# Kernel tuning notes

Hardware: AMD Instinct MI355X
Metric: run time of the kernel (lower is better)

## Reference

```python
import jax, jax.numpy as jnp
import numpy as np

BATCH, K_DIM, SEQ_L = 8, 1, 2048
D_MODEL, D_STATE, KCH = 256, 64, 2  # 64 complex states == d_state 128 real; 2 kernel channels (bidirectional)


def setup_inputs() -> dict:
    key = jax.random.key(0)
    ks = jax.random.split(key, 12)
    H, N = D_MODEL, D_STATE
    s = 1.0 / np.sqrt(H)
    # log-uniform timestep in [1e-3, 1e-1] as in S4 init
    dt = jnp.exp(jax.random.uniform(ks[2], (H,)) * (np.log(0.1) - np.log(0.001)) + np.log(0.001))
    return {
        "x": jax.random.normal(ks[0], (BATCH, H, K_DIM, SEQ_L), jnp.float32),
        "t": jax.random.normal(ks[1], (BATCH, 1, H), jnp.float32),
        "W_t": jax.random.normal(ks[3], (H, H)) * s,
        "b_t": jnp.zeros((H,)),
        "ln_g": jnp.ones((H,)),
        "ln_b": jnp.zeros((H,)),
        "log_dt": jnp.log(dt),
        "log_A_real": jnp.log(0.5 * jnp.ones((H, N))),
        "A_imag": jnp.tile(np.pi * jnp.arange(N, dtype=np.float32), (H, 1)),
        "B_re": jnp.ones((H, N)),
        "B_im": jnp.zeros((H, N)),
        "C_re": jax.random.normal(ks[4], (KCH, H, N)) * np.sqrt(0.5),
        "C_im": jax.random.normal(ks[5], (KCH, H, N)) * np.sqrt(0.5),
        "D": jax.random.normal(ks[6], (H,)),
        "W_out": jax.random.normal(ks[7], (H, H)) * s,
        "b_out": jnp.zeros((H,)),
        "W1": jax.random.normal(ks[8], (H, H)) * s,
        "b1": jnp.zeros((H,)),
        "W2": jax.random.normal(ks[9], (H, H)) * s,
        "b2": jnp.zeros((H,)),
    }


def _s4_kernel(log_dt, log_A_real, A_imag, B_re, B_im, C_re, C_im, L):
    # Diagonal SSM convolution kernel (ZOH discretization), 2 channels for bidirectional
    dt = jnp.exp(log_dt)[:, None]                      # (H,1)
    A = -jnp.exp(log_A_real) + 1j * A_imag             # (H,N)
    B = B_re + 1j * B_im                               # (H,N)
    C = C_re + 1j * C_im                               # (KCH,H,N)
    dtA = dt * A
    dB = B * (jnp.exp(dtA) - 1.0) / A                  # ZOH input discretization
    V = jnp.exp(dtA[:, :, None] * jnp.arange(L))       # (H,N,L) Vandermonde of dA^l
    return 2.0 * jnp.einsum('chn,hnl->chl', C * dB, V).real  # (KCH,H,L)


def _s4_layer(u, ln_g, ln_b, log_dt, log_A_real, A_imag, B_re, B_im, C_re, C_im, D, W_out, b_out):
    # u: (B*, H, L). Pre-LayerNorm over channels, S4 FFT conv, D skip, GELU, out proj, residual.
    mu = jnp.mean(u, axis=1, keepdims=True)
    var = jnp.var(u, axis=1, keepdims=True)
    z = (u - mu) / jnp.sqrt(var + 1e-5) * ln_g[:, None] + ln_b[:, None]
    L = u.shape[-1]
    k = _s4_kernel(log_dt, log_A_real, A_imag, B_re, B_im, C_re, C_im, L)
    # bidirectional: causal kernel + time-reversed kernel, combined at length 2L
    k_bi = jnp.pad(k[0], ((0, 0), (0, L))) + jnp.pad(k[1][:, ::-1], ((0, 0), (L, 0)))  # (H,2L)
    kf = jnp.fft.rfft(k_bi, n=2 * L)                   # (H,L+1)
    zf = jnp.fft.rfft(z, n=2 * L)                      # (B*,H,L+1)
    y = jnp.fft.irfft(zf * kf[None], n=2 * L)[..., :L]
    y = y + z * D[:, None]
    y = jax.nn.gelu(y, approximate=False)
    y = jnp.einsum('oh,bhl->bol', W_out, y) + b_out[:, None]  # transposed output linear
    return y + u


def reference(x, t, W_t, b_t, ln_g, ln_b, log_dt, log_A_real, A_imag, B_re, B_im, C_re, C_im, D, W_out, b_out, W1, b1, W2, b2):
    b, c, k, l = x.shape
    tt = jnp.einsum('boc,dc->bod', t, W_t) + b_t       # time_linear: (b,1,H)
    s4_in = x + tt[:, 0, :, None, None]                # 'b 1 c -> b c 1 1' broadcast
    u = s4_in.transpose(0, 2, 1, 3).reshape(b * k, c, l)  # 'b c k l -> (b k) c l'
    out = _s4_layer(u, ln_g, ln_b, log_dt, log_A_real, A_imag, B_re, B_im, C_re, C_im, D, W_out, b_out)
    out = out.reshape(b, k, c, l).transpose(0, 2, 1, 3)   # '(b k) c l -> b c k l'
    g = jnp.tanh(out) * jax.nn.sigmoid(out)            # WaveNet-style gate
    out1 = jnp.einsum('oc,bckl->bokl', W1, g) + b1[None, :, None, None]  # 1x1 conv2d
    out2 = jnp.einsum('oc,bckl->bokl', W2, g) + b2[None, :, None, None]
    return (out1 + x, out2)
```

## Files before the change

kernel.cpp:

```cpp
#include <hip/hip_runtime.h>
#include <math.h>

#define LL 2048
#define HH 256
#define BB 8
#define NN 64
#define HN (HH*NN)
#define ELEMS (BB*HH*LL)

typedef __attribute__((ext_vector_type(8))) short bf16x8v;
typedef __attribute__((ext_vector_type(4))) float f32x4v;

static inline __device__ ushort f2b_rne(float f) {
  uint u = __float_as_uint(f);
  return (ushort)((u + 0x7fffu + ((u >> 16) & 1u)) >> 16);
}
static inline __device__ float b2f(ushort u) { return __uint_as_float((uint)u << 16); }
#define UNPK(u, lo, hi) { lo = __uint_as_float((u)<<16); hi = __uint_as_float((u)&0xffff0000u); }

__global__ __launch_bounds__(256) void init_kernel(
    const float* __restrict__ t, const float* __restrict__ W_t, const float* __restrict__ b_t,
    const float* __restrict__ log_dt, const float* __restrict__ log_A_real,
    const float* __restrict__ A_imag,
    const float* __restrict__ B_re, const float* __restrict__ B_im,
    const float* __restrict__ C_re, const float* __restrict__ C_im,
    const float* __restrict__ Dp,
    const float* __restrict__ Wo, const float* __restrict__ W1, const float* __restrict__ W2,
    float* __restrict__ P, float* __restrict__ tt,
    ushort* __restrict__ Wob, ushort* __restrict__ W1b, ushort* __restrict__ W2b,
    ushort* __restrict__ Mc, ushort* __restrict__ Vc, ushort* __restrict__ Uc,
    float* __restrict__ rT) {
  int blk = blockIdx.x;
  int tid = threadIdx.x;
  if (blk < BB) {
    int b = blk, h = tid;
    float s = b_t[h];
    const float* trow = t + b*HH;
    const float* wrow = W_t + h*HH;
    for (int c = 0; c < HH; ++c) s = fmaf(trow[c], wrow[c], s);
    tt[b*HH + h] = s;
    return;
  }
  if (blk < BB + 192) {
    int q = blk - BB;
    int m = q >> 6;
    int i = (q & 63)*1024 + tid*4;
    const float* src = (m==0) ? Wo : (m==1 ? W1 : W2);
    ushort* dst = (m==0) ? Wob : (m==1 ? W1b : W2b);
    float4 v = *reinterpret_cast<const float4*>(src + i);
    union { ushort us[4]; uint2 u2; } pk;
    pk.us[0] = f2b_rne(v.x); pk.us[1] = f2b_rne(v.y);
    pk.us[2] = f2b_rne(v.z); pk.us[3] = f2b_rne(v.w);
    *reinterpret_cast<uint2*>(dst + i) = pk.u2;
    return;
  }
  int h = blk - (BB + 192);
  __shared__ float RRe[65][64], RIm[65][64];
  __shared__ float K0[64], K1[64];
  __shared__ float W0r[64], W0i[64], W1r[64], W1i[64];
  float dt = expf(log_dt[h]);
  for (int idx = tid; idx < 65*64; idx += 256) {
    int d = idx >> 6, n = idx & 63;
    float are = -expf(log_A_real[h*64+n]);
    float aim = A_imag[h*64+n];
    float ang = dt*aim*(float)d;
    float mag = expf(dt*are*(float)d);
    RRe[d][n] = mag * cosf(ang);
    RIm[d][n] = mag * sinf(ang);
  }
  __syncthreads();
  if (tid < 64) {
    int n = tid, gid = h*64 + n;
    float are = -expf(log_A_real[gid]);
    float aim = A_imag[gid];
    float rre = RRe[1][n], rim = RIm[1][n];
    float inv  = 1.0f / (are*are + aim*aim);
    float m_re = rre - 1.0f, m_im = rim;
    float q_re = (m_re*are + m_im*aim) * inv;
    float q_im = (m_im*are - m_re*aim) * inv;
    float bre = B_re[gid], bim = B_im[gid];
    float db_re = q_re*bre - q_im*bim;
    float db_im = q_re*bim + q_im*bre;
    float c0r = C_re[gid],      c0i = C_im[gid];
    float c1r = C_re[HN + gid], c1i = C_im[HN + gid];
    float w0r = 2.0f*(c0r*db_re - c0i*db_im), w0i = 2.0f*(c0r*db_im + c0i*db_re);
    float w1r = 2.0f*(c1r*db_re - c1i*db_im), w1i = 2.0f*(c1r*db_im + c1i*db_re);
    W0r[n] = w0r; W0i[n] = w0i; W1r[n] = w1r; W1i[n] = w1i;
    P[gid]        = w0r;
    P[HN + gid]   = w0i;
    P[2*HN + gid] = w1r;
    P[3*HN + gid] = w1i;
    rT[gid*2]   = RRe[64][n];
    rT[gid*2+1] = RIm[64][n];
  }
  __syncthreads();
  if (tid < 128) {
    int d = tid & 63; bool c1 = tid >= 64;
    float s = 0.f;
    if (!c1) for (int n = 0; n < 64; ++n) s += W0r[n]*RRe[d][n] - W0i[n]*RIm[d][n];
    else     for (int n = 0; n < 64; ++n) s += W1r[n]*RRe[d][n] - W1i[n]*RIm[d][n];
    if (c1) K1[d] = s; else K0[d] = s;
  }
  __syncthreads();
  float dh = Dp[h];
  for (int idx = tid; idx < 4096; idx += 256) {
    int i = idx >> 6, j = idx & 63;
    float v = (i > j) ? K0[i-j] : (i < j ? K1[j-i-1] : (K0[0] + dh));
    Mc[(size_t)h*4096 + idx] = f2b_rne(v);
  }
  for (int idx = tid; idx < 256*64; idx += 256) {
    int row = idx >> 6, j = idx & 63;
    int n = (row >> 1) & 63;
    bool im = row & 1, bwd = row >= 128;
    int d = bwd ? j : 63-j;
    Vc[(size_t)h*16384 + idx] = f2b_rne(im ? RIm[d][n] : RRe[d][n]);
  }
  for (int idx = tid; idx < 64*256; idx += 256) {
    int i = idx >> 8, col = idx & 255;
    int n = (col >> 1) & 63;
    bool im = col & 1, bwd = col >= 128;
    int d = bwd ? 63-i : i+1;
    Uc[(size_t)h*16384 + idx] = f2b_rne(im ? -RIm[d][n] : RRe[d][n]);
  }
}

__global__ __launch_bounds__(256) void lnz_kernel(
    const float* __restrict__ x, const float* __restrict__ tt,
    const float* __restrict__ ln_g, const float* __restrict__ ln_b,
    ushort* __restrict__ zb, ushort* __restrict__ xt) {
  int b  = blockIdx.x >> 6;
  int l0 = (blockIdx.x & 63) * 32;
  int tid = threadIdx.x;
  int r8 = tid >> 3;
  int c  = tid & 7;
  __shared__ ushort XS[256][36];
  __shared__ float SS[32][33], SS2[32][33];
  __shared__ float MU[32], RS[32];
  float s[4] = {0.f,0.f,0.f,0.f}, s2[4] = {0.f,0.f,0.f,0.f};
  #pragma unroll
  for (int it = 0; it < 8; ++it) {
    int h = it*32 + r8;
    float ttv = tt[b*HH + h];
    float vv[4];
    *reinterpret_cast<float4*>(vv) =
        *reinterpret_cast<const float4*>(x + (size_t)(b*HH + h)*LL + l0 + c*4);
    #pragma unroll
    for (int j = 0; j < 4; ++j) {
      float w = vv[j] + ttv;
      s[j] += w; s2[j] = fmaf(w, w, s2[j]);
      XS[h][c*4 + j] = f2b_rne(w);
    }
  }
  #pragma unroll
  for (int j = 0; j < 4; ++j) { SS[c*4+j][r8] = s[j]; SS2[c*4+j][r8] = s2[j]; }
  __syncthreads();
  if (tid < 32) {
    float a = 0.f, a2 = 0.f;
    #pragma unroll
    for (int p = 0; p < 32; ++p) { a += SS[tid][p]; a2 += SS2[tid][p]; }
    float m = a * (1.0f/HH);
    float var = a2 * (1.0f/HH) - m*m;
    MU[tid] = m;
    RS[tid] = 1.0f / sqrtf(var + 1e-5f);
  }
  __syncthreads();
  #pragma unroll
  for (int it = 0; it < 8; ++it) {
    int h = it*32 + r8;
    float gg = ln_g[h], bb2 = ln_b[h];
    uint2 u2 = *reinterpret_cast<const uint2*>(&XS[h][c*4]);
    float v0, v1, v2, v3;
    UNPK(u2.x, v0, v1); UNPK(u2.y, v2, v3);
    int l = c*4;
    float z0 = (v0 - MU[l])   * RS[l]   * gg + bb2;
    float z1 = (v1 - MU[l+1]) * RS[l+1] * gg + bb2;
    float z2 = (v2 - MU[l+2]) * RS[l+2] * gg + bb2;
    float z3 = (v3 - MU[l+3]) * RS[l+3] * gg + bb2;
    uint2 zo;
    zo.x = (uint)f2b_rne(z0) | ((uint)f2b_rne(z1) << 16);
    zo.y = (uint)f2b_rne(z2) | ((uint)f2b_rne(z3) << 16);
    size_t off = (size_t)(b*HH + h)*LL + l0 + l;
    *reinterpret_cast<uint2*>(zb + off) = zo;
    *reinterpret_cast<uint2*>(xt + off) = u2;
  }
}

__global__ __launch_bounds__(512) void ssm_all(
    const ushort* __restrict__ zb, const ushort* __restrict__ Vc,
    const ushort* __restrict__ Mc, const ushort* __restrict__ Uc,
    const float* __restrict__ P, const float* __restrict__ rT,
    ushort* __restrict__ g) {
  int b0 = blockIdx.x * 4;
  int h  = blockIdx.y;
  int tid = threadIdx.x, wid = tid >> 6, lane = tid & 63;
  int row16 = lane & 15, kg = lane >> 4;
  __shared__ ushort G[128][260];

  {
    int comp0 = (wid >> 1)*64, bct = (wid & 1)*64;
    f32x4v acc[4][4];
    #pragma unroll
    for (int fm = 0; fm < 4; ++fm)
      #pragma unroll
      for (int fn = 0; fn < 4; ++fn) acc[fm][fn] = (f32x4v){0.f,0.f,0.f,0.f};
    #pragma unroll
    for (int k0 = 0; k0 < 64; k0 += 32) {
      bf16x8v a[4], bv[4];
      #pragma unroll
      for (int fm = 0; fm < 4; ++fm)
        a[fm] = *reinterpret_cast<const bf16x8v*>(
            Vc + (size_t)h*16384 + (comp0 + fm*16 + row16)*64 + k0 + kg*8);
      #pragma unroll
      for (int fn = 0; fn < 4; ++fn) {
        int bc = bct + fn*16 + row16; int b = b0 + (bc >> 5), c = bc & 31;
        bv[fn] = *reinterpret_cast<const bf16x8v*>(
            zb + ((size_t)(b*HH + h))*LL + c*64 + k0 + kg*8);
      }
      #pragma unroll
      for (int fm = 0; fm < 4; ++fm)
        #pragma unroll
        for (int fn = 0; fn < 4; ++fn)
          acc[fm][fn] = __builtin_amdgcn_mfma_f32_16x16x32_bf16(a[fm], bv[fn], acc[fm][fn], 0,0,0);
    }
    #pragma unroll
    for (int fm = 0; fm < 4; ++fm)
      #pragma unroll
      for (int fn = 0; fn < 4; ++fn) {
        int bc = bct + fn*16 + row16;
        int comp = comp0 + fm*16 + kg*4;
        union { ushort us[4]; uint2 u2; } pk;
        #pragma unroll
        for (int r = 0; r < 4; ++r) pk.us[r] = f2b_rne(acc[fm][fn][r]);
        *reinterpret_cast<uint2*>(&G[bc][comp]) = pk.u2;
      }
  }
  __syncthreads();

  {
    int bloc = wid & 3, dir = wid >> 2;
    int n = lane;
    float w_re = dir ? P[2*HN + h*64+n] : P[h*64+n];
    float w_im = dir ? P[3*HN + h*64+n] : P[HN + h*64+n];
    float rtr = rT[(h*64+n)*2], rti = rT[(h*64+n)*2+1];
    float sre = 0.f, sim = 0.f;
    if (dir == 0) {
      for (int c = 0; c < 32; ++c) {
        uint* slot = reinterpret_cast<uint*>(&G[bloc*32 + c][2*n]);
        uint gg = *slot;
        float ure = w_re*sre - w_im*sim;
        float uim = w_re*sim + w_im*sre;
        *slot = (uint)f2b_rne(ure) | ((uint)f2b_rne(uim) << 16);
        float gre, gim; UNPK(gg, gre, gim);
        float nre = rtr*sre - rti*sim + gre;
        float nim = rtr*sim + rti*sre + gim;
        sre = nre; sim = nim;
      }
    } else {
      for (int c = 31; c >= 0; --c) {
        uint* slot = reinterpret_cast<uint*>(&G[bloc*32 + c][128 + 2*n]);
        uint gg = *slot;
        float ure = w_re*sre - w_im*sim;
        float uim = w_re*sim + w_im*sre;
        *slot = (uint)f2b_rne(ure) | ((uint)f2b_rne(uim) << 16);
        float gre, gim; UNPK(gg, gre, gim);
        float nre = rtr*sre - rti*sim + gre;
        float nim = rtr*sim + rti*sre + gim;
        sre = nre; sim = nim;
      }
    }
  }
  __syncthreads();

  {
    int i0 = (wid & 3)*16, bct = (wid >> 2)*64;
    f32x4v acc[4];
    #pragma unroll
    for (int fn = 0; fn < 4; ++fn) acc[fn] = (f32x4v){0.f,0.f,0.f,0.f};
    #pragma unroll
    for (int k0 = 0; k0 < 64; k0 += 32) {
      bf16x8v a = *reinterpret_cast<const bf16x8v*>(
          Mc + (size_t)h*4096 + (i0 + row16)*64 + k0 + kg*8);
      #pragma unroll
      for (int fn = 0; fn < 4; ++fn) {
        int bc = bct + fn*16 + row16; int b = b0 + (bc >> 5), c = bc & 31;
        bf16x8v bv = *reinterpret_cast<const bf16x8v*>(
            zb + ((size_t)(b*HH + h))*LL + c*64 + k0 + kg*8);
        acc[fn] = __builtin_amdgcn_mfma_f32_16x16x32_bf16(a, bv, acc[fn], 0,0,0);
      }
    }
    #pragma unroll
    for (int k0 = 0; k0 < 256; k0 += 32) {
      bf16x8v a = *reinterpret_cast<const bf16x8v*>(
          Uc + (size_t)h*16384 + (i0 + row16)*256 + k0 + kg*8);
      #pragma unroll
      for (int fn = 0; fn < 4; ++fn) {
        bf16x8v bv = *reinterpret_cast<const bf16x8v*>(&G[bct + fn*16 + row16][k0 + kg*8]);
        acc[fn] = __builtin_amdgcn_mfma_f32_16x16x32_bf16(a, bv, acc[fn], 0,0,0);
      }
    }
    #pragma unroll
    for (int fn = 0; fn < 4; ++fn) {
      int bc = bct + fn*16 + row16; int b = b0 + (bc >> 5), c = bc & 31;
      union { ushort us[4]; uint2 u2; } pk;
      #pragma unroll
      for (int r = 0; r < 4; ++r) {
        float v = acc[fn][r];
        float ge = 0.5f * v * (1.0f + erff(v * 0.70710678118654752f));
        pk.us[r] = f2b_rne(ge);
      }
      *reinterpret_cast<uint2*>(&g[((size_t)(b*HH + h))*LL + c*64 + i0 + kg*4]) = pk.u2;
    }
  }
}

__global__ __launch_bounds__(256, 2) void fused_out(
    const ushort* __restrict__ g, const ushort* __restrict__ Wob,
    const ushort* __restrict__ W1b, const ushort* __restrict__ W2b,
    const float* __restrict__ b_out, const float* __restrict__ b1v,
    const float* __restrict__ b2v, const ushort* __restrict__ xt,
    const float* __restrict__ tt,
    float* __restrict__ out1, float* __restrict__ out2) {
  int l0 = blockIdx.x * 32;
  int b  = blockIdx.y;
  int tid = threadIdx.x, wid = tid >> 6, lane = tid & 63;
  int row16 = lane & 15, kg = lane >> 4;
  int o0 = wid * 64;

  __shared__ ushort Tg[32][274];
  __shared__ ushort X[256][38];

  bf16x8v wA[8][4];
  #pragma unroll
  for (int k8 = 0; k8 < 8; ++k8)
    #pragma unroll
    for (int fo = 0; fo < 4; ++fo)
      wA[k8][fo] = *reinterpret_cast<const bf16x8v*>(
          Wob + (size_t)(o0 + fo*16 + row16)*HH + k8*32 + kg*8);

  {
    const ushort* gsrc = g + (size_t)b*HH*LL + l0;
    int cq = tid & 7;
    #pragma unroll
    for (int p = 0; p < 8; ++p) {
      int h = p*32 + (tid >> 3);
      uint2 v = *reinterpret_cast<const uint2*>(gsrc + (size_t)h*LL + cq*4);
      union { uint2 u2; ushort us[4]; } pk; pk.u2 = v;
      #pragma unroll
      for (int j = 0; j < 4; ++j) Tg[cq*4 + j][h] = pk.us[j];
    }
  }
  {
    const ushort* xsrc = xt + (size_t)b*HH*LL + l0;
    int cq = tid & 7;
    #pragma unroll
    for (int p = 0; p < 8; ++p) {
      int o = p*32 + (tid >> 3);
      uint2 v = *reinterpret_cast<const uint2*>(xsrc + (size_t)o*LL + cq*4);
      *reinterpret_cast<uint2*>(&X[o][cq*4]) = v;
    }
  }
  float biasA[4][4];
  #pragma unroll
  for (int fo = 0; fo < 4; ++fo)
    #pragma unroll
    for (int r = 0; r < 4; ++r)
      biasA[fo][r] = b_out[o0 + fo*16 + kg*4 + r];
  __syncthreads();

  f32x4v accA[4][2];
  #pragma unroll
  for (int fo = 0; fo < 4; ++fo)
    #pragma unroll
    for (int fl = 0; fl < 2; ++fl) accA[fo][fl] = (f32x4v){0.f,0.f,0.f,0.f};
  #pragma unroll
  for (int k8 = 0; k8 < 8; ++k8) {
    bf16x8v bb[2];
    #pragma unroll
    for (int fl = 0; fl < 2; ++fl)
      bb[fl] = *reinterpret_cast<const bf16x8v*>(&Tg[fl*16+row16][k8*32 + kg*8]);
    #pragma unroll
    for (int fo = 0; fo < 4; ++fo)
      #pragma unroll
      for (int fl = 0; fl < 2; ++fl)
        accA[fo][fl] = __builtin_amdgcn_mfma_f32_16x16x32_bf16(wA[k8][fo], bb[fl], accA[fo][fl], 0,0,0);
  }
  bf16x8v w1[8][4];
  #pragma unroll
  for (int k8 = 0; k8 < 8; ++k8)
    #pragma unroll
    for (int fo = 0; fo < 4; ++fo)
      w1[k8][fo] = *reinterpret_cast<const bf16x8v*>(
          W1b + (size_t)(o0 + fo*16 + row16)*HH + k8*32 + kg*8);
  uint2 gw[4][2];
  #pragma unroll
  for (int fo = 0; fo < 4; ++fo)
    #pragma unroll
    for (int fl = 0; fl < 2; ++fl) {
      union { ushort us[4]; uint2 u2; } pk;
      #pragma unroll
      for (int r = 0; r < 4; ++r) {
        int o = o0 + fo*16 + kg*4 + r;
        int l = fl*16 + row16;
        float v = accA[fo][fl][r] + biasA[fo][r] + b2f(X[o][l]);
        float gate = tanhf(v) * (1.0f/(1.0f + expf(-v)));
        pk.us[r] = f2b_rne(gate);
      }
      gw[fo][fl] = pk.u2;
    }
  __syncthreads();
  #pragma unroll
  for (int fo = 0; fo < 4; ++fo)
    #pragma unroll
    for (int fl = 0; fl < 2; ++fl)
      *reinterpret_cast<uint2*>(&Tg[fl*16+row16][o0 + fo*16 + kg*4]) = gw[fo][fl];
  __syncthreads();

  {
    f32x4v p[2][4];
    #pragma unroll
    for (int fl = 0; fl < 2; ++fl)
      #pragma unroll
      for (int fo = 0; fo < 4; ++fo) p[fl][fo] = (f32x4v){0.f,0.f,0.f,0.f};
    #pragma unroll
    for (int k8 = 0; k8 < 8; ++k8) {
      bf16x8v bb[2];
      #pragma unroll
      for (int fl = 0; fl < 2; ++fl)
        bb[fl] = *reinterpret_cast<const bf16x8v*>(&Tg[fl*16+row16][k8*32 + kg*8]);
      #pragma unroll
      for (int fl = 0; fl < 2; ++fl)
        #pragma unroll
        for (int fo = 0; fo < 4; ++fo)
          p[fl][fo] = __builtin_amdgcn_mfma_f32_16x16x32_bf16(bb[fl], w1[k8][fo], p[fl][fo], 0,0,0);
    }
    #pragma unroll
    for (int k8 = 0; k8 < 8; ++k8)
      #pragma unroll
      for (int fo = 0; fo < 4; ++fo)
        wA[k8][fo] = *reinterpret_cast<const bf16x8v*>(
            W2b + (size_t)(o0 + fo*16 + row16)*HH + k8*32 + kg*8);
    #pragma unroll
    for (int fl = 0; fl < 2; ++fl)
      #pragma unroll
      for (int fo = 0; fo < 4; ++fo) {
        int o  = o0 + fo*16 + row16;
        int lb = fl*16 + kg*4;
        float bias = b1v[o] - tt[b*HH + o];
        uint2 xv = *reinterpret_cast<const uint2*>(&X[o][lb]);
        float x0, x1, x2, x3;
        UNPK(xv.x, x0, x1); UNPK(xv.y, x2, x3);
        float4 v;
        v.x = p[fl][fo][0] + bias + x0;
        v.y = p[fl][fo][1] + bias + x1;
        v.z = p[fl][fo][2] + bias + x2;
        v.w = p[fl][fo][3] + bias + x3;
        *reinterpret_cast<float4*>(&out1[((size_t)(b*HH + o))*LL + l0 + lb]) = v;
      }
  }
  {
    f32x4v q[2][4];
    #pragma unroll
    for (int fl = 0; fl < 2; ++fl)
      #pragma unroll
      for (int fo = 0; fo < 4; ++fo) q[fl][fo] = (f32x4v){0.f,0.f,0.f,0.f};
    #pragma unroll
    for (int k8 = 0; k8 < 8; ++k8) {
      bf16x8v bb[2];
      #pragma unroll
      for (int fl = 0; fl < 2; ++fl)
        bb[fl] = *reinterpret_cast<const bf16x8v*>(&Tg[fl*16+row16][k8*32 + kg*8]);
      #pragma unroll
      for (int fl = 0; fl < 2; ++fl)
        #pragma unroll
        for (int fo = 0; fo < 4; ++fo)
          q[fl][fo] = __builtin_amdgcn_mfma_f32_16x16x32_bf16(bb[fl], wA[k8][fo], q[fl][fo], 0,0,0);
    }
    #pragma unroll
    for (int fl = 0; fl < 2; ++fl)
      #pragma unroll
      for (int fo = 0; fo < 4; ++fo) {
        int o  = o0 + fo*16 + row16;
        int lb = fl*16 + kg*4;
        float bias = b2v[o];
        float4 v;
        v.x = q[fl][fo][0] + bias;
        v.y = q[fl][fo][1] + bias;
        v.z = q[fl][fo][2] + bias;
        v.w = q[fl][fo][3] + bias;
        *reinterpret_cast<float4*>(&out2[((size_t)(b*HH + o))*LL + l0 + lb]) = v;
      }
  }
}

extern "C" void kernel_launch(void* const* d_in, const int* in_sizes, int n_in,
                              void* d_out, int out_size, void* d_ws, size_t ws_size,
                              hipStream_t stream) {
  const float* x    = (const float*)d_in[0];
  const float* t    = (const float*)d_in[1];
  const float* W_t  = (const float*)d_in[2];
  const float* b_t  = (const float*)d_in[3];
  const float* ln_g = (const float*)d_in[4];
  const float* ln_b = (const float*)d_in[5];
  const float* log_dt = (const float*)d_in[6];
  const float* log_A_real = (const float*)d_in[7];
  const float* A_imag = (const float*)d_in[8];
  const float* B_re = (const float*)d_in[9];
  const float* B_im = (const float*)d_in[10];
  const float* C_re = (const float*)d_in[11];
  const float* C_im = (const float*)d_in[12];
  const float* Dp   = (const float*)d_in[13];
  const float* W_out= (const float*)d_in[14];
  const float* b_out= (const float*)d_in[15];
  const float* W1   = (const float*)d_in[16];
  const float* b1   = (const float*)d_in[17];
  const float* W2   = (const float*)d_in[18];
  const float* b2   = (const float*)d_in[19];

  float* out1 = (float*)d_out;
  float* out2 = out1 + ELEMS;

  float* P    = (float*)d_ws;
  float* tt   = P + 4*HN;
  float* rT   = tt + BB*HH;
  ushort* zb  = (ushort*)(rT + 2*HN);
  ushort* Mc  = zb + ELEMS;
  ushort* Vc  = Mc + (size_t)4096*HH;
  ushort* Uc  = Vc + (size_t)16384*HH;
  ushort* g   = Uc + (size_t)16384*HH;
  ushort* Wob = g + ELEMS;
  ushort* W1b = Wob + HH*HH;
  ushort* W2b = W1b + HH*HH;
  ushort* xt  = W2b + HH*HH;

  init_kernel<<<BB + 192 + HH, 256, 0, stream>>>(
      t, W_t, b_t, log_dt, log_A_real, A_imag, B_re, B_im, C_re, C_im, Dp,
      W_out, W1, W2, P, tt, Wob, W1b, W2b, Mc, Vc, Uc, rT);
  lnz_kernel<<<BB*64, 256, 0, stream>>>(x, tt, ln_g, ln_b, zb, xt);
  ssm_all<<<dim3(2, HH), 512, 0, stream>>>(zb, Vc, Mc, Uc, P, rT, g);
  fused_out<<<dim3(LL/32, BB), 256, 0, stream>>>(g, Wob, W1b, W2b, b_out, b1, b2,
                                                 xt, tt, out1, out2);
}
```

Before: 102.3 us.

## Split fused output kernel into gate kernel and separate dual-GEMM output kernel

```diff
diff --git a/kernel.cpp b/kernel.cpp
--- a/kernel.cpp
+++ b/kernel.cpp
@@ -313,13 +313,10 @@
   }
 }
 
-__global__ __launch_bounds__(256, 2) void fused_out(
+__global__ __launch_bounds__(256, 2) void gate_k(
     const ushort* __restrict__ g, const ushort* __restrict__ Wob,
-    const ushort* __restrict__ W1b, const ushort* __restrict__ W2b,
-    const float* __restrict__ b_out, const float* __restrict__ b1v,
-    const float* __restrict__ b2v, const ushort* __restrict__ xt,
-    const float* __restrict__ tt,
-    float* __restrict__ out1, float* __restrict__ out2) {
+    const float* __restrict__ b_out, const ushort* __restrict__ xt,
+    ushort* __restrict__ gate) {
   int l0 = blockIdx.x * 32;
   int b  = blockIdx.y;
   int tid = threadIdx.x, wid = tid >> 6, lane = tid & 63;
@@ -348,10 +345,7 @@
       #pragma unroll
       for (int j = 0; j < 4; ++j) Tg[cq*4 + j][h] = pk.us[j];
     }
-  }
-  {
     const ushort* xsrc = xt + (size_t)b*HH*LL + l0;
-    int cq = tid & 7;
     #pragma unroll
     for (int p = 0; p < 8; ++p) {
       int o = p*32 + (tid >> 3);
@@ -384,111 +378,85 @@
       for (int fl = 0; fl < 2; ++fl)
         accA[fo][fl] = __builtin_amdgcn_mfma_f32_16x16x32_bf16(wA[k8][fo], bb[fl], accA[fo][fl], 0,0,0);
   }
-  bf16x8v w1[8][4];
-  #pragma unroll
-  for (int k8 = 0; k8 < 8; ++k8)
-    #pragma unroll
-    for (int fo = 0; fo < 4; ++fo)
-      w1[k8][fo] = *reinterpret_cast<const bf16x8v*>(
-          W1b + (size_t)(o0 + fo*16 + row16)*HH + k8*32 + kg*8);
-  uint2 gw[4][2];
   #pragma unroll
   for (int fo = 0; fo < 4; ++fo)
     #pragma unroll
     for (int fl = 0; fl < 2; ++fl) {
       union { ushort us[4]; uint2 u2; } pk;
+      int l = fl*16 + row16;
       #pragma unroll
       for (int r = 0; r < 4; ++r) {
         int o = o0 + fo*16 + kg*4 + r;
-        int l = fl*16 + row16;
         float v = accA[fo][fl][r] + biasA[fo][r] + b2f(X[o][l]);
-        float gate = tanhf(v) * (1.0f/(1.0f + expf(-v)));
-        pk.us[r] = f2b_rne(gate);
-      }
-      gw[fo][fl] = pk.u2;
-    }
-  __syncthreads();
-  #pragma unroll
-  for (int fo = 0; fo < 4; ++fo)
-    #pragma unroll
-    for (int fl = 0; fl < 2; ++fl)
-      *reinterpret_cast<uint2*>(&Tg[fl*16+row16][o0 + fo*16 + kg*4]) = gw[fo][fl];
-  __syncthreads();
-
-  {
-    f32x4v p[2][4];
-    #pragma unroll
-    for (int fl = 0; fl < 2; ++fl)
-      #pragma unroll
-      for (int fo = 0; fo < 4; ++fo) p[fl][fo] = (f32x4v){0.f,0.f,0.f,0.f};
-    #pragma unroll
-    for (int k8 = 0; k8 < 8; ++k8) {
-      bf16x8v bb[2];
-      #pragma unroll
-      for (int fl = 0; fl < 2; ++fl)
-        bb[fl] = *reinterpret_cast<const bf16x8v*>(&Tg[fl*16+row16][k8*32 + kg*8]);
-      #pragma unroll
-      for (int fl = 0; fl < 2; ++fl)
-        #pragma unroll
-        for (int fo = 0; fo < 4; ++fo)
-          p[fl][fo] = __builtin_amdgcn_mfma_f32_16x16x32_bf16(bb[fl], w1[k8][fo], p[fl][fo], 0,0,0);
-    }
-    #pragma unroll
-    for (int k8 = 0; k8 < 8; ++k8)
-      #pragma unroll
-      for (int fo = 0; fo < 4; ++fo)
-        wA[k8][fo] = *reinterpret_cast<const bf16x8v*>(
-            W2b + (size_t)(o0 + fo*16 + row16)*HH + k8*32 + kg*8);
-    #pragma unroll
-    for (int fl = 0; fl < 2; ++fl)
-      #pragma unroll
-      for (int fo = 0; fo < 4; ++fo) {
-        int o  = o0 + fo*16 + row16;
-        int lb = fl*16 + kg*4;
-        float bias = b1v[o] - tt[b*HH + o];
-        uint2 xv = *reinterpret_cast<const uint2*>(&X[o][lb]);
-        float x0, x1, x2, x3;
-        UNPK(xv.x, x0, x1); UNPK(xv.y, x2, x3);
-        float4 v;
-        v.x = p[fl][fo][0] + bias + x0;
-        v.y = p[fl][fo][1] + bias + x1;
-        v.z = p[fl][fo][2] + bias + x2;
-        v.w = p[fl][fo][3] + bias + x3;
-        *reinterpret_cast<float4*>(&out1[((size_t)(b*HH + o))*LL + l0 + lb]) = v;
-      }
-  }
-  {
-    f32x4v q[2][4];
-    #pragma unroll
-    for (int fl = 0; fl < 2; ++fl)
-      #pragma unroll
-      for (int fo = 0; fo < 4; ++fo) q[fl][fo] = (f32x4v){0.f,0.f,0.f,0.f};
-    #pragma unroll
-    for (int k8 = 0; k8 < 8; ++k8) {
-      bf16x8v bb[2];
-      #pragma unroll
-      for (int fl = 0; fl < 2; ++fl)
-        bb[fl] = *reinterpret_cast<const bf16x8v*>(&Tg[fl*16+row16][k8*32 + kg*8]);
-      #pragma unroll
-      for (int fl = 0; fl < 2; ++fl)
-        #pragma unroll
-        for (int fo = 0; fo < 4; ++fo)
-          q[fl][fo] = __builtin_amdgcn_mfma_f32_16x16x32_bf16(bb[fl], wA[k8][fo], q[fl][fo], 0,0,0);
-    }
-    #pragma unroll
-    for (int fl = 0; fl < 2; ++fl)
-      #pragma unroll
-      for (int fo = 0; fo < 4; ++fo) {
-        int o  = o0 + fo*16 + row16;
-        int lb = fl*16 + kg*4;
-        float bias = b2v[o];
-        float4 v;
-        v.x = q[fl][fo][0] + bias;
-        v.y = q[fl][fo][1] + bias;
-        v.z = q[fl][fo][2] + bias;
-        v.w = q[fl][fo][3] + bias;
-        *reinterpret_cast<float4*>(&out2[((size_t)(b*HH + o))*LL + l0 + lb]) = v;
-      }
+        float gt = tanhf(v) * (1.0f/(1.0f + expf(-v)));
+        pk.us[r] = f2b_rne(gt);
+      }
+      *reinterpret_cast<uint2*>(&gate[((size_t)b*LL + l0 + l)*HH + o0 + fo*16 + kg*4]) = pk.u2;
+    }
+}
+
+__global__ __launch_bounds__(256) void out_k(
+    const ushort* __restrict__ gate, const ushort* __restrict__ W1b,
+    const ushort* __restrict__ W2b,
+    const float* __restrict__ b1v, const float* __restrict__ b2v,
+    const ushort* __restrict__ xt, const float* __restrict__ tt,
+    float* __restrict__ out1, float* __restrict__ out2) {
+  int lr = blockIdx.x, ot = blockIdx.y, b = blockIdx.z;
+  int tid = threadIdx.x, wid = tid >> 6, lane = tid & 63;
+  int row16 = lane & 15, kg = lane >> 4;
+  int lbase = lr*512 + wid*128;
+  int o0 = ot*32;
+
+  f32x4v a1[2][8], a2[2][8];
+  #pragma unroll
+  for (int fo = 0; fo < 2; ++fo)
+    #pragma unroll
+    for (int lf = 0; lf < 8; ++lf) { a1[fo][lf] = (f32x4v){0.f,0.f,0.f,0.f}; a2[fo][lf] = a1[fo][lf]; }
+
+  for (int k0 = 0; k0 < HH; k0 += 32) {
+    bf16x8v w1f[2], w2f[2];
+    #pragma unroll
+    for (int fo = 0; fo < 2; ++fo) {
+      w1f[fo] = *reinterpret_cast<const bf16x8v*>(W1b + (size_t)(o0+fo*16+row16)*HH + k0 + kg*8);
+      w2f[fo] = *reinterpret_cast<const bf16x8v*>(W2b + (size_t)(o0+fo*16+row16)*HH + k0 + kg*8);
+    }
+    #pragma unroll
+    for (int lf = 0; lf < 8; ++lf) {
+      bf16x8v gf = *reinterpret_cast<const bf16x8v*>(
+          gate + ((size_t)b*LL + lbase + lf*16 + row16)*HH + k0 + kg*8);
+      #pragma unroll
+      for (int fo = 0; fo < 2; ++fo) {
+        a1[fo][lf] = __builtin_amdgcn_mfma_f32_16x16x32_bf16(gf, w1f[fo], a1[fo][lf], 0,0,0);
+        a2[fo][lf] = __builtin_amdgcn_mfma_f32_16x16x32_bf16(gf, w2f[fo], a2[fo][lf], 0,0,0);
+      }
+    }
+  }
+
+  #pragma unroll
+  for (int fo = 0; fo < 2; ++fo) {
+    int o = o0 + fo*16 + row16;
+    float bias1 = b1v[o] - tt[b*HH + o];
+    float bias2 = b2v[o];
+    #pragma unroll
+    for (int lf = 0; lf < 8; ++lf) {
+      int l = lbase + lf*16 + kg*4;
+      size_t off = ((size_t)(b*HH + o))*LL + l;
+      uint2 xv = *reinterpret_cast<const uint2*>(xt + off);
+      float x0, x1, x2, x3;
+      UNPK(xv.x, x0, x1); UNPK(xv.y, x2, x3);
+      float4 v1;
+      v1.x = a1[fo][lf][0] + bias1 + x0;
+      v1.y = a1[fo][lf][1] + bias1 + x1;
+      v1.z = a1[fo][lf][2] + bias1 + x2;
+      v1.w = a1[fo][lf][3] + bias1 + x3;
+      *reinterpret_cast<float4*>(&out1[off]) = v1;
+      float4 v2;
+      v2.x = a2[fo][lf][0] + bias2;
+      v2.y = a2[fo][lf][1] + bias2;
+      v2.z = a2[fo][lf][2] + bias2;
+      v2.w = a2[fo][lf][3] + bias2;
+      *reinterpret_cast<float4*>(&out2[off]) = v2;
+    }
   }
 }
 
@@ -531,12 +499,13 @@
   ushort* W1b = Wob + HH*HH;
   ushort* W2b = W1b + HH*HH;
   ushort* xt  = W2b + HH*HH;
+  ushort* gate = zb;
 
   init_kernel<<<BB + 192 + HH, 256, 0, stream>>>(
       t, W_t, b_t, log_dt, log_A_real, A_imag, B_re, B_im, C_re, C_im, Dp,
       W_out, W1, W2, P, tt, Wob, W1b, W2b, Mc, Vc, Uc, rT);
   lnz_kernel<<<BB*64, 256, 0, stream>>>(x, tt, ln_g, ln_b, zb, xt);
   ssm_all<<<dim3(2, HH), 512, 0, stream>>>(zb, Vc, Mc, Uc, P, rT, g);
-  fused_out<<<dim3(LL/32, BB), 256, 0, stream>>>(g, Wob, W1b, W2b, b_out, b1, b2,
-                                                 xt, tt, out1, out2);
-}
+  gate_k<<<dim3(LL/32, BB), 256, 0, stream>>>(g, Wob, b_out, xt, gate);
+  out_k<<<dim3(4, 8, BB), 256, 0, stream>>>(gate, W1b, W2b, b1, b2, xt, tt, out1, out2);
+}
```

New measurement: 108.4 us. 1.06x slower.
